# Performance work log

Hardware: AMD Instinct MI355X
Metric: run time of the kernel (lower is better)

## Reference

```python
import jax, jax.numpy as jnp
import numpy as np

RHO, MU, DT = 1.0, 0.1, 4.0
AX_X, AX_Y = -1, -2  # x = last axis, y = second-to-last


def first_derivative(f, ax, scheme):
    # unit grid spacing; boundary wrap is irrelevant since [1:-1,1:-1] is sliced off
    if scheme == 'left':
        return f - jnp.roll(f, 1, ax)
    if scheme == 'right':
        return jnp.roll(f, -1, ax) - f
    return 0.5 * (jnp.roll(f, -1, ax) - jnp.roll(f, 1, ax))  # central


def vel_map(f, ax, side):
    # staggered-grid interpolation of velocity to neighboring face
    if side == 'left':
        return 0.5 * (f + jnp.roll(f, 1, ax))
    return 0.5 * (f + jnp.roll(f, -1, ax))


def laplacian(f):
    return (jnp.roll(f, 1, AX_X) + jnp.roll(f, -1, AX_X)
            + jnp.roll(f, 1, AX_Y) + jnp.roll(f, -1, AX_Y) - 4.0 * f)


def setup_inputs() -> dict:
    key = jax.random.key(0)
    k1, k2, k3, k4 = jax.random.split(key, 4)
    B, H, W = 8, 1024, 1024
    return {
        'v_old': jax.random.normal(k1, (B, 2, H, W), dtype=jnp.float32),
        'v_new': jax.random.normal(k2, (B, 2, H, W), dtype=jnp.float32),
        'p_new': jax.random.normal(k3, (B, 1, H, W), dtype=jnp.float32),
        'flow_mask_mac': jax.random.randint(k4, (B, 1, H, W), 0, 2).astype(jnp.int32),
    }


def reference(v_old, v_new, p_new, flow_mask_mac):
    mask = flow_mask_mac.astype(v_old.dtype)
    v = 0.5 * (v_new + v_old)  # integration == 'imex'

    u_old, w_old = v_old[:, 0:1], v_old[:, 1:2]
    u_new, w_new = v_new[:, 0:1], v_new[:, 1:2]
    u, w = v[:, 0:1], v[:, 1:2]

    # x-momentum residual (channel 1)
    res_x = mask * (RHO * ((w_new - w_old) / DT
                           + w * first_derivative(w, AX_X, 'central')
                           + 0.5 * (vel_map(u, AX_X, 'left') * first_derivative(w, AX_Y, 'left')
                                    + vel_map(u, AX_X, 'right') * first_derivative(w, AX_Y, 'right')))
                    + first_derivative(p_new, AX_X, 'left')
                    - MU * laplacian(w))

    # y-momentum residual (channel 0)
    res_y = mask * (RHO * ((u_new - u_old) / DT
                           + u * first_derivative(u, AX_Y, 'central')
                           + 0.5 * (vel_map(w, AX_Y, 'left') * first_derivative(u, AX_X, 'left')
                                    + vel_map(w, AX_Y, 'right') * first_derivative(u, AX_X, 'right')))
                    + first_derivative(p_new, AX_Y, 'left')
                    - MU * laplacian(u))

    loss_x = jnp.mean(jnp.square(res_x)[:, :, 1:-1, 1:-1], axis=(1, 2, 3))
    loss_y = jnp.mean(jnp.square(res_y)[:, :, 1:-1, 1:-1], axis=(1, 2, 3))
    return loss_x + loss_y  # shape [B]
```

## Files before the change

kernel.cpp:

```cpp
#include <hip/hip_runtime.h>


#define NS_H 1024
#define NS_W 1024
#define RPB 4
#define NBY 256
#define PARTS_PER_B NBY

__device__ __forceinline__ float4 ld4(const float* p) { return *(const float4*)p; }
__device__ __forceinline__ int4  ld4i(const int* p)   { return *(const int4*)p; }
__device__ __forceinline__ float4 avg4(float4 a, float4 b) {
    return make_float4(0.5f*(a.x+b.x), 0.5f*(a.y+b.y), 0.5f*(a.z+b.z), 0.5f*(a.w+b.w));
}
__device__ __forceinline__ float4 sub4(float4 a, float4 b) {
    return make_float4(a.x-b.x, a.y-b.y, a.z-b.z, a.w-b.w);
}

__global__ __launch_bounds__(256, 3) void ns_loss_partial(
    const float* __restrict__ v_old,
    const float* __restrict__ v_new,
    const float* __restrict__ p,
    const int*   __restrict__ mask,
    float* __restrict__ ws)
{
    const int blkp = blockIdx.x;
    const int lg   = (blkp & 7) * (NBY) + (blkp >> 3) % NBY + ((blkp >> 3) / NBY) * 0;
    const int lg2  = (blkp & 7) * 256 + (blkp >> 3);
    const int b    = lg2 / NBY;
    const int cy   = lg2 % NBY;
    const int y0   = 1 + cy * RPB;

    const size_t hw = (size_t)NS_H * NS_W;
    const float* uo = v_old + (size_t)b * 2 * hw;
    const float* wo = uo + hw;
    const float* un = v_new + (size_t)b * 2 * hw;
    const float* wn = un + hw;
    const float* pb = p    + (size_t)b * hw;
    const int*   mb = mask + (size_t)b * hw;

    const int tid  = (int)threadIdx.x;
    const int lane = tid & 63;
    const int wid  = tid >> 6;
    const int x0   = tid * 4;
    const bool has_r = (x0 + 4 < NS_W);

    int R1 = y0,     R2 = y0 + 1, R3 = y0 + 2, R4 = y0 + 3, R5 = y0 + 4;
    if (R3 > 1023) R3 = 1023;
    if (R4 > 1023) R4 = 1023;
    if (R5 > 1023) R5 = 1023;
    const int o0 = (y0 - 1) * NS_W + x0;
    const int o1 = R1 * NS_W + x0;
    const int o2 = R2 * NS_W + x0;
    const int o3 = R3 * NS_W + x0;
    const int o4 = R4 * NS_W + x0;
    const int o5 = R5 * NS_W + x0;

    float4 un0 = ld4(un + o0), uo0 = ld4(uo + o0);
    float4 un1 = ld4(un + o1), uo1 = ld4(uo + o1);
    float4 un2 = ld4(un + o2), uo2 = ld4(uo + o2);
    float4 un3 = ld4(un + o3), uo3 = ld4(uo + o3);
    float4 un4 = ld4(un + o4), uo4 = ld4(uo + o4);
    float4 un5 = ld4(un + o5), uo5 = ld4(uo + o5);
    float4 wn0 = ld4(wn + o0), wo0 = ld4(wo + o0);
    float4 wn1 = ld4(wn + o1), wo1 = ld4(wo + o1);
    float4 wn2 = ld4(wn + o2), wo2 = ld4(wo + o2);
    float4 wn3 = ld4(wn + o3), wo3 = ld4(wo + o3);
    float4 wn4 = ld4(wn + o4), wo4 = ld4(wo + o4);
    float4 wn5 = ld4(wn + o5), wo5 = ld4(wo + o5);
    float4 P[5];
    P[0] = ld4(pb + o0); P[1] = ld4(pb + o1); P[2] = ld4(pb + o2);
    P[3] = ld4(pb + o3); P[4] = ld4(pb + o4);
    int4 M[4];
    M[0] = ld4i(mb + o1); M[1] = ld4i(mb + o2);
    M[2] = ld4i(mb + o3); M[3] = ld4i(mb + o4);

    float4 U[6], W[6], DU[4], DW[4];
    U[0] = avg4(un0, uo0); W[0] = avg4(wn0, wo0);
    U[1] = avg4(un1, uo1); W[1] = avg4(wn1, wo1); DU[0] = sub4(un1, uo1); DW[0] = sub4(wn1, wo1);
    U[2] = avg4(un2, uo2); W[2] = avg4(wn2, wo2); DU[1] = sub4(un2, uo2); DW[1] = sub4(wn2, wo2);
    U[3] = avg4(un3, uo3); W[3] = avg4(wn3, wo3); DU[2] = sub4(un3, uo3); DW[2] = sub4(wn3, wo3);
    U[4] = avg4(un4, uo4); W[4] = avg4(wn4, wo4); DU[3] = sub4(un4, uo4); DW[3] = sub4(wn4, wo4);
    U[5] = avg4(un5, uo5); W[5] = avg4(wn5, wo5);

    __shared__ float edge[4][4][5];
    if (lane == 63) {
        #pragma unroll
        for (int k = 0; k < 4; ++k) {
            edge[wid][k][0] = U[k+1].w; edge[wid][k][1] = W[k+1].w; edge[wid][k][2] = P[k+1].w;
        }
    }
    if (lane == 0) {
        #pragma unroll
        for (int k = 0; k < 4; ++k) {
            edge[wid][k][3] = U[k+1].x; edge[wid][k][4] = W[k+1].x;
        }
    }
    __syncthreads();

    float acc = 0.f;

    #pragma unroll
    for (int k = 0; k < 4; ++k) {
        const float rowvalid = (y0 + k <= NS_H - 2) ? 1.f : 0.f;

        float ul = __shfl_up(U[k+1].w, 1), wl = __shfl_up(W[k+1].w, 1), pl = __shfl_up(P[k+1].w, 1);
        if (lane == 0 && wid > 0) {
            ul = edge[wid-1][k][0]; wl = edge[wid-1][k][1]; pl = edge[wid-1][k][2];
        }
        float ur = __shfl_down(U[k+1].x, 1), wr = __shfl_down(W[k+1].x, 1);
        if (lane == 63 && wid < 3) {
            ur = edge[wid+1][k][3]; wr = edge[wid+1][k][4];
        }
        if (!has_r) { ur = 0.f; wr = 0.f; }

        const float uc[6]  = {ul, U[k+1].x, U[k+1].y, U[k+1].z, U[k+1].w, ur};
        const float wcv[6] = {wl, W[k+1].x, W[k+1].y, W[k+1].z, W[k+1].w, wr};
        const float uym[4] = {U[k].x, U[k].y, U[k].z, U[k].w};
        const float uyp[4] = {U[k+2].x, U[k+2].y, U[k+2].z, U[k+2].w};
        const float wym[4] = {W[k].x, W[k].y, W[k].z, W[k].w};
        const float wyp[4] = {W[k+2].x, W[k+2].y, W[k+2].z, W[k+2].w};
        const float du[4]  = {DU[k].x, DU[k].y, DU[k].z, DU[k].w};
        const float dw[4]  = {DW[k].x, DW[k].y, DW[k].z, DW[k].w};
        const float pcv[5] = {pl, P[k+1].x, P[k+1].y, P[k+1].z, P[k+1].w};
        const float pym[4] = {P[k].x, P[k].y, P[k].z, P[k].w};
        const int   mm[4]  = {M[k].x, M[k].y, M[k].z, M[k].w};

        #pragma unroll
        for (int j = 0; j < 4; ++j) {
            const int x = x0 + j;
            const float m = ((x >= 1 && x <= NS_W - 2) ? (float)mm[j] : 0.f) * rowvalid;
            const float u_cc = uc[j+1],  u_xm = uc[j],  u_xp = uc[j+2];
            const float w_cc = wcv[j+1], w_xm = wcv[j], w_xp = wcv[j+2];

            float res_x =
                dw[j] * 0.25f
              + w_cc * 0.5f * (w_xp - w_xm)
              + 0.5f * ( 0.5f * (u_cc + u_xm) * (w_cc   - wym[j])
                       + 0.5f * (u_cc + u_xp) * (wyp[j] - w_cc  ) )
              + (pcv[j+1] - pcv[j])
              - 0.1f * (w_xm + w_xp + wym[j] + wyp[j] - 4.f * w_cc);

            float res_y =
                du[j] * 0.25f
              + u_cc * 0.5f * (uyp[j] - uym[j])
              + 0.5f * ( 0.5f * (w_cc + wym[j]) * (u_cc - u_xm)
                       + 0.5f * (w_cc + wyp[j]) * (u_xp - u_cc) )
              + (pcv[j+1] - pym[j])
              - 0.1f * (u_xm + u_xp + uym[j] + uyp[j] - 4.f * u_cc);

            acc += m * (res_x * res_x + res_y * res_y);
        }
    }

    #pragma unroll
    for (int off = 32; off > 0; off >>= 1)
        acc += __shfl_down(acc, off);

    __shared__ float smem[4];
    if (lane == 0) smem[wid] = acc;
    __syncthreads();

    if (tid == 0)
        ws[lg2] = smem[0] + smem[1] + smem[2] + smem[3];
}

__global__ __launch_bounds__(256) void ns_loss_reduce(
    const float* __restrict__ ws, float* __restrict__ out)
{
    const int b = blockIdx.x;
    float acc = 0.f;
    for (int i = threadIdx.x; i < PARTS_PER_B; i += 256)
        acc += ws[b * PARTS_PER_B + i];

    #pragma unroll
    for (int off = 32; off > 0; off >>= 1)
        acc += __shfl_down(acc, off);

    __shared__ float smem[4];
    const int lane = threadIdx.x & 63;
    const int wid  = threadIdx.x >> 6;
    if (lane == 0) smem[wid] = acc;
    __syncthreads();

    if (threadIdx.x == 0) {
        const float inv = 1.0f / ((float)(NS_H - 2) * (float)(NS_W - 2));
        out[b] = (smem[0] + smem[1] + smem[2] + smem[3]) * inv;
    }
}

extern "C" void kernel_launch(void* const* d_in, const int* in_sizes, int n_in,
                              void* d_out, int out_size, void* d_ws, size_t ws_size,
                              hipStream_t stream) {
    const float* v_old = (const float*)d_in[0];
    const float* v_new = (const float*)d_in[1];
    const float* p_new = (const float*)d_in[2];
    const int*   msk   = (const int*)d_in[3];
    float* out = (float*)d_out;
    float* ws  = (float*)d_ws;

    const int B = out_size;

    ns_loss_partial<<<dim3(B * NBY), dim3(256), 0, stream>>>(v_old, v_new, p_new, msk, ws);
    ns_loss_reduce<<<dim3(B), dim3(256), 0, stream>>>(ws, out);
}
```

Measured before the change: 212.9 us.

## Stream rows through LDS ring buffer with async global-to-LDS loads

Each block now covers a 32-row by 512-column strip and walks down it row by row. Rows are staged into a 4-slot shared-memory ring with global_load_lds, and hand-placed waitcnt/barriers overlap the next row's loads with the current row's stencil. This is meant to remove the redundant halo-row reads of the old 4-row blocks and to hide load latency. In exchange it launches far fewer, smaller blocks and adds barriers per row, which may limit memory parallelism.

```diff
diff --git a/kernel.cpp b/kernel.cpp
--- a/kernel.cpp
+++ b/kernel.cpp
@@ -3,12 +3,19 @@
 
 #define NS_H 1024
 #define NS_W 1024
-#define RPB 4
-#define NBY 256
-#define PARTS_PER_B NBY
-
-__device__ __forceinline__ float4 ld4(const float* p) { return *(const float4*)p; }
-__device__ __forceinline__ int4  ld4i(const int* p)   { return *(const int4*)p; }
+#define RY   32
+#define NCH  32
+#define NBLK 512
+#define PARTS_PER_B 64
+
+#define GL16(gp, lp) __builtin_amdgcn_global_load_lds( \
+    (const __attribute__((address_space(1))) void*)(gp), \
+    (__attribute__((address_space(3))) void*)(lp), 16, 0, 0)
+#define GL4(gp, lp) __builtin_amdgcn_global_load_lds( \
+    (const __attribute__((address_space(1))) void*)(gp), \
+    (__attribute__((address_space(3))) void*)(lp), 4, 0, 0)
+
+__device__ __forceinline__ float4 rd4(const float* p) { return *(const float4*)p; }
 __device__ __forceinline__ float4 avg4(float4 a, float4 b) {
     return make_float4(0.5f*(a.x+b.x), 0.5f*(a.y+b.y), 0.5f*(a.z+b.z), 0.5f*(a.w+b.w));
 }
@@ -16,7 +23,7 @@
     return make_float4(a.x-b.x, a.y-b.y, a.z-b.z, a.w-b.w);
 }
 
-__global__ __launch_bounds__(256, 3) void ns_loss_partial(
+__global__ __launch_bounds__(128) void ns_loss_partial(
     const float* __restrict__ v_old,
     const float* __restrict__ v_new,
     const float* __restrict__ p,
@@ -24,11 +31,13 @@
     float* __restrict__ ws)
 {
     const int blkp = blockIdx.x;
-    const int lg   = (blkp & 7) * (NBY) + (blkp >> 3) % NBY + ((blkp >> 3) / NBY) * 0;
-    const int lg2  = (blkp & 7) * 256 + (blkp >> 3);
-    const int b    = lg2 / NBY;
-    const int cy   = lg2 % NBY;
-    const int y0   = 1 + cy * RPB;
+    const int lg   = (blkp & 7) * (NBLK / 8) + (blkp >> 3);
+    const int b    = lg >> 6;
+    const int rem  = lg & 63;
+    const int c    = rem >> 1;
+    const int t    = rem & 1;
+    const int y0   = 1 + c * RY;
+    const int gx   = t * 512;
 
     const size_t hw = (size_t)NS_H * NS_W;
     const float* uo = v_old + (size_t)b * 2 * hw;
@@ -36,99 +45,129 @@
     const float* un = v_new + (size_t)b * 2 * hw;
     const float* wn = un + hw;
     const float* pb = p    + (size_t)b * hw;
-    const int*   mb = mask + (size_t)b * hw;
-
-    const int tid  = (int)threadIdx.x;
-    const int lane = tid & 63;
-    const int wid  = tid >> 6;
-    const int x0   = tid * 4;
-    const bool has_r = (x0 + 4 < NS_W);
-
-    int R1 = y0,     R2 = y0 + 1, R3 = y0 + 2, R4 = y0 + 3, R5 = y0 + 4;
-    if (R3 > 1023) R3 = 1023;
-    if (R4 > 1023) R4 = 1023;
-    if (R5 > 1023) R5 = 1023;
-    const int o0 = (y0 - 1) * NS_W + x0;
-    const int o1 = R1 * NS_W + x0;
-    const int o2 = R2 * NS_W + x0;
-    const int o3 = R3 * NS_W + x0;
-    const int o4 = R4 * NS_W + x0;
-    const int o5 = R5 * NS_W + x0;
-
-    float4 un0 = ld4(un + o0), uo0 = ld4(uo + o0);
-    float4 un1 = ld4(un + o1), uo1 = ld4(uo + o1);
-    float4 un2 = ld4(un + o2), uo2 = ld4(uo + o2);
-    float4 un3 = ld4(un + o3), uo3 = ld4(uo + o3);
-    float4 un4 = ld4(un + o4), uo4 = ld4(uo + o4);
-    float4 un5 = ld4(un + o5), uo5 = ld4(uo + o5);
-    float4 wn0 = ld4(wn + o0), wo0 = ld4(wo + o0);
-    float4 wn1 = ld4(wn + o1), wo1 = ld4(wo + o1);
-    float4 wn2 = ld4(wn + o2), wo2 = ld4(wo + o2);
-    float4 wn3 = ld4(wn + o3), wo3 = ld4(wo + o3);
-    float4 wn4 = ld4(wn + o4), wo4 = ld4(wo + o4);
-    float4 wn5 = ld4(wn + o5), wo5 = ld4(wo + o5);
-    float4 P[5];
-    P[0] = ld4(pb + o0); P[1] = ld4(pb + o1); P[2] = ld4(pb + o2);
-    P[3] = ld4(pb + o3); P[4] = ld4(pb + o4);
-    int4 M[4];
-    M[0] = ld4i(mb + o1); M[1] = ld4i(mb + o2);
-    M[2] = ld4i(mb + o3); M[3] = ld4i(mb + o4);
-
-    float4 U[6], W[6], DU[4], DW[4];
-    U[0] = avg4(un0, uo0); W[0] = avg4(wn0, wo0);
-    U[1] = avg4(un1, uo1); W[1] = avg4(wn1, wo1); DU[0] = sub4(un1, uo1); DW[0] = sub4(wn1, wo1);
-    U[2] = avg4(un2, uo2); W[2] = avg4(wn2, wo2); DU[1] = sub4(un2, uo2); DW[1] = sub4(wn2, wo2);
-    U[3] = avg4(un3, uo3); W[3] = avg4(wn3, wo3); DU[2] = sub4(un3, uo3); DW[2] = sub4(wn3, wo3);
-    U[4] = avg4(un4, uo4); W[4] = avg4(wn4, wo4); DU[3] = sub4(un4, uo4); DW[3] = sub4(wn4, wo4);
-    U[5] = avg4(un5, uo5); W[5] = avg4(wn5, wo5);
-
-    __shared__ float edge[4][4][5];
-    if (lane == 63) {
-        #pragma unroll
-        for (int k = 0; k < 4; ++k) {
-            edge[wid][k][0] = U[k+1].w; edge[wid][k][1] = W[k+1].w; edge[wid][k][2] = P[k+1].w;
-        }
-    }
-    if (lane == 0) {
-        #pragma unroll
-        for (int k = 0; k < 4; ++k) {
-            edge[wid][k][3] = U[k+1].x; edge[wid][k][4] = W[k+1].x;
-        }
-    }
-    __syncthreads();
+    const float* mbf = (const float*)(mask + (size_t)b * hw);
+
+    const int tid = (int)threadIdx.x;
+    const int wv  = tid >> 6;
+    const int ln  = tid & 63;
+    const int q0  = tid * 4;
+
+    __shared__ float ring[4][6][512];
+    __shared__ float es[4][64];
+    __shared__ float sred[2];
+
+    auto stage_set = [&](int slot, int gr) {
+        const size_t rb = (size_t)gr * NS_W + gx;
+        if (wv == 0) {
+            GL16(un + rb +       (size_t)ln*4, &ring[slot][0][0]);
+            GL16(un + rb + 256 + (size_t)ln*4, &ring[slot][0][256]);
+            GL16(uo + rb +       (size_t)ln*4, &ring[slot][1][0]);
+            GL16(uo + rb + 256 + (size_t)ln*4, &ring[slot][1][256]);
+            GL16(wn + rb +       (size_t)ln*4, &ring[slot][2][0]);
+            GL16(wn + rb + 256 + (size_t)ln*4, &ring[slot][2][256]);
+        } else {
+            GL16(wo + rb +       (size_t)ln*4, &ring[slot][3][0]);
+            GL16(wo + rb + 256 + (size_t)ln*4, &ring[slot][3][256]);
+            GL16(pb + rb +       (size_t)ln*4, &ring[slot][4][0]);
+            GL16(pb + rb + 256 + (size_t)ln*4, &ring[slot][4][256]);
+            GL16(mbf + rb +       (size_t)ln*4, &ring[slot][5][0]);
+            GL16(mbf + rb + 256 + (size_t)ln*4, &ring[slot][5][256]);
+            const int xl = (gx == 0) ? 0 : gx - 1;
+            const int xr = (gx + 512 <= NS_W - 1) ? gx + 512 : NS_W - 1;
+            const size_t rowb = (size_t)gr * NS_W;
+            const float* ep;
+            switch (ln) {
+                case 0: ep = un + rowb + xl; break;
+                case 1: ep = uo + rowb + xl; break;
+                case 2: ep = wn + rowb + xl; break;
+                case 3: ep = wo + rowb + xl; break;
+                case 4: ep = pb + rowb + xl; break;
+                case 5: ep = un + rowb + xr; break;
+                case 6: ep = uo + rowb + xr; break;
+                case 7: ep = wn + rowb + xr; break;
+                case 8: ep = wo + rowb + xr; break;
+                default: ep = pb + rowb + gx; break;
+            }
+            GL4(ep, &es[slot][0]);
+        }
+    };
+
+    stage_set(0, y0 - 1);
+    stage_set(1, y0);
+    stage_set(2, y0 + 1);
+    __builtin_amdgcn_sched_barrier(0);
 
     float acc = 0.f;
 
-    #pragma unroll
-    for (int k = 0; k < 4; ++k) {
-        const float rowvalid = (y0 + k <= NS_H - 2) ? 1.f : 0.f;
-
-        float ul = __shfl_up(U[k+1].w, 1), wl = __shfl_up(W[k+1].w, 1), pl = __shfl_up(P[k+1].w, 1);
-        if (lane == 0 && wid > 0) {
-            ul = edge[wid-1][k][0]; wl = edge[wid-1][k][1]; pl = edge[wid-1][k][2];
-        }
-        float ur = __shfl_down(U[k+1].x, 1), wr = __shfl_down(W[k+1].x, 1);
-        if (lane == 63 && wid < 3) {
-            ur = edge[wid+1][k][3]; wr = edge[wid+1][k][4];
-        }
-        if (!has_r) { ur = 0.f; wr = 0.f; }
-
-        const float uc[6]  = {ul, U[k+1].x, U[k+1].y, U[k+1].z, U[k+1].w, ur};
-        const float wcv[6] = {wl, W[k+1].x, W[k+1].y, W[k+1].z, W[k+1].w, wr};
-        const float uym[4] = {U[k].x, U[k].y, U[k].z, U[k].w};
-        const float uyp[4] = {U[k+2].x, U[k+2].y, U[k+2].z, U[k+2].w};
-        const float wym[4] = {W[k].x, W[k].y, W[k].z, W[k].w};
-        const float wyp[4] = {W[k+2].x, W[k+2].y, W[k+2].z, W[k+2].w};
-        const float du[4]  = {DU[k].x, DU[k].y, DU[k].z, DU[k].w};
-        const float dw[4]  = {DW[k].x, DW[k].y, DW[k].z, DW[k].w};
-        const float pcv[5] = {pl, P[k+1].x, P[k+1].y, P[k+1].z, P[k+1].w};
-        const float pym[4] = {P[k].x, P[k].y, P[k].z, P[k].w};
-        const int   mm[4]  = {M[k].x, M[k].y, M[k].z, M[k].w};
+    for (int r = 0; r < RY; ++r) {
+        __builtin_amdgcn_s_barrier();
+        __builtin_amdgcn_sched_barrier(0);
+
+        if (r < RY - 1) {
+            int gr = y0 + r + 2; if (gr > NS_H - 1) gr = NS_H - 1;
+            stage_set((r + 3) & 3, gr);
+            __builtin_amdgcn_sched_barrier(0);
+            if (wv == 0) asm volatile("s_waitcnt vmcnt(6)" ::: "memory");
+            else         asm volatile("s_waitcnt vmcnt(7)" ::: "memory");
+        } else {
+            asm volatile("s_waitcnt vmcnt(0)" ::: "memory");
+        }
+        __builtin_amdgcn_s_barrier();
+        __builtin_amdgcn_sched_barrier(0);
+
+        const int sm = r & 3, sc = (r + 1) & 3, sp = (r + 2) & 3;
+        const float rv = (y0 + r <= NS_H - 2) ? 1.f : 0.f;
+
+        float4 unc = rd4(&ring[sc][0][q0]), uoc = rd4(&ring[sc][1][q0]);
+        float4 wnc = rd4(&ring[sc][2][q0]), woc = rd4(&ring[sc][3][q0]);
+        float4 unm = rd4(&ring[sm][0][q0]), uom = rd4(&ring[sm][1][q0]);
+        float4 wnm = rd4(&ring[sm][2][q0]), wom = rd4(&ring[sm][3][q0]);
+        float4 unp = rd4(&ring[sp][0][q0]), uop = rd4(&ring[sp][1][q0]);
+        float4 wnp = rd4(&ring[sp][2][q0]), wop = rd4(&ring[sp][3][q0]);
+        float4 pc4 = rd4(&ring[sc][4][q0]);
+        float4 pm4 = rd4(&ring[sm][4][q0]);
+        float4 mk4 = rd4(&ring[sc][5][q0]);
+
+        float4 u_cv = avg4(unc, uoc), w_cv = avg4(wnc, woc);
+        float4 duv  = sub4(unc, uoc), dwv  = sub4(wnc, woc);
+        float4 u_mv = avg4(unm, uom), w_mv = avg4(wnm, wom);
+        float4 u_pv = avg4(unp, uop), w_pv = avg4(wnp, wop);
+
+        float ul, wl, plv, urr, wrr;
+        if (q0 == 0) {
+            ul  = 0.5f * (es[sc][0] + es[sc][1]);
+            wl  = 0.5f * (es[sc][2] + es[sc][3]);
+            plv = es[sc][4];
+        } else {
+            ul  = 0.5f * (ring[sc][0][q0-1] + ring[sc][1][q0-1]);
+            wl  = 0.5f * (ring[sc][2][q0-1] + ring[sc][3][q0-1]);
+            plv = ring[sc][4][q0-1];
+        }
+        if (q0 == 508) {
+            urr = 0.5f * (es[sc][5] + es[sc][6]);
+            wrr = 0.5f * (es[sc][7] + es[sc][8]);
+        } else {
+            urr = 0.5f * (ring[sc][0][q0+4] + ring[sc][1][q0+4]);
+            wrr = 0.5f * (ring[sc][2][q0+4] + ring[sc][3][q0+4]);
+        }
+
+        const float uc[6]  = {ul, u_cv.x, u_cv.y, u_cv.z, u_cv.w, urr};
+        const float wcv[6] = {wl, w_cv.x, w_cv.y, w_cv.z, w_cv.w, wrr};
+        const float uym[4] = {u_mv.x, u_mv.y, u_mv.z, u_mv.w};
+        const float uyp[4] = {u_pv.x, u_pv.y, u_pv.z, u_pv.w};
+        const float wym[4] = {w_mv.x, w_mv.y, w_mv.z, w_mv.w};
+        const float wyp[4] = {w_pv.x, w_pv.y, w_pv.z, w_pv.w};
+        const float du[4]  = {duv.x, duv.y, duv.z, duv.w};
+        const float dw[4]  = {dwv.x, dwv.y, dwv.z, dwv.w};
+        const float pcv[5] = {plv, pc4.x, pc4.y, pc4.z, pc4.w};
+        const float pym[4] = {pm4.x, pm4.y, pm4.z, pm4.w};
+        const unsigned mm[4] = {__float_as_uint(mk4.x), __float_as_uint(mk4.y),
+                                __float_as_uint(mk4.z), __float_as_uint(mk4.w)};
 
         #pragma unroll
         for (int j = 0; j < 4; ++j) {
-            const int x = x0 + j;
-            const float m = ((x >= 1 && x <= NS_W - 2) ? (float)mm[j] : 0.f) * rowvalid;
+            const int x = gx + q0 + j;
+            const float m = ((x >= 1 && x <= NS_W - 2) ? (float)mm[j] : 0.f) * rv;
             const float u_cc = uc[j+1],  u_xm = uc[j],  u_xp = uc[j+2];
             const float w_cc = wcv[j+1], w_xm = wcv[j], w_xp = wcv[j+2];
 
@@ -156,35 +195,26 @@
     for (int off = 32; off > 0; off >>= 1)
         acc += __shfl_down(acc, off);
 
-    __shared__ float smem[4];
-    if (lane == 0) smem[wid] = acc;
+    if (ln == 0) sred[wv] = acc;
     __syncthreads();
 
     if (tid == 0)
-        ws[lg2] = smem[0] + smem[1] + smem[2] + smem[3];
-}
-
-__global__ __launch_bounds__(256) void ns_loss_reduce(
+        ws[lg] = sred[0] + sred[1];
+}
+
+__global__ __launch_bounds__(64) void ns_loss_reduce(
     const float* __restrict__ ws, float* __restrict__ out)
 {
     const int b = blockIdx.x;
-    float acc = 0.f;
-    for (int i = threadIdx.x; i < PARTS_PER_B; i += 256)
-        acc += ws[b * PARTS_PER_B + i];
+    float a = ws[b * PARTS_PER_B + threadIdx.x];
 
     #pragma unroll
     for (int off = 32; off > 0; off >>= 1)
-        acc += __shfl_down(acc, off);
-
-    __shared__ float smem[4];
-    const int lane = threadIdx.x & 63;
-    const int wid  = threadIdx.x >> 6;
-    if (lane == 0) smem[wid] = acc;
-    __syncthreads();
+        a += __shfl_down(a, off);
 
     if (threadIdx.x == 0) {
         const float inv = 1.0f / ((float)(NS_H - 2) * (float)(NS_W - 2));
-        out[b] = (smem[0] + smem[1] + smem[2] + smem[3]) * inv;
+        out[b] = a * inv;
     }
 }
 
@@ -200,6 +230,6 @@
 
     const int B = out_size;
 
-    ns_loss_partial<<<dim3(B * NBY), dim3(256), 0, stream>>>(v_old, v_new, p_new, msk, ws);
-    ns_loss_reduce<<<dim3(B), dim3(256), 0, stream>>>(ws, out);
-}
+    ns_loss_partial<<<dim3(NBLK), dim3(128), 0, stream>>>(v_old, v_new, p_new, msk, ws);
+    ns_loss_reduce<<<dim3(B), dim3(64), 0, stream>>>(ws, out);
+}
```

After: 204.2 us. 4.1% less time.
